# Optimization experiments

Hardware: AMD Instinct MI355X
Metric: run time of the kernel (lower is better)

The kernel has to match this reference:

```python
import jax, jax.numpy as jnp
import numpy as np

N = 100000      # nodes
E = 2500000     # edges
DIN, H, DOUT = 3, 32, 4
EPS = 1e-5

def _lin(k, i, o):
    kw, kb = jax.random.split(k)
    lim = 1.0 / np.sqrt(i)
    W = jax.random.uniform(kw, (i, o), jnp.float32, -lim, lim)
    b = jax.random.uniform(kb, (o,), jnp.float32, -lim, lim)
    return W, b

def setup_inputs():
    key = jax.random.key(0)
    ks = jax.random.split(key, 12)
    x = jax.random.normal(ks[0], (N, DIN), jnp.float32)
    edge_index = jax.random.randint(ks[1], (2, E), 0, N, dtype=jnp.int32)
    w_in1, b_in1 = _lin(ks[2], DIN, H)
    w_in2, b_in2 = _lin(ks[3], H, H)
    gamma = jnp.ones((H,), jnp.float32)
    beta = jnp.zeros((H,), jnp.float32)
    wg1, bg1 = _lin(ks[4], H, H)
    wg2, bg2 = _lin(ks[5], H, H)
    wg3, bg3 = _lin(ks[6], H, H)
    wo1, bo1 = _lin(ks[7], H, H)
    wo2, bo2 = _lin(ks[8], H, H)
    wo3, bo3 = _lin(ks[9], H, DOUT)
    return dict(x=x, w_in1=w_in1, b_in1=b_in1, w_in2=w_in2, b_in2=b_in2,
                gamma=gamma, beta=beta,
                wg1=wg1, bg1=bg1, wg2=wg2, bg2=bg2, wg3=wg3, bg3=bg3,
                wo1=wo1, bo1=bo1, wo2=wo2, bo2=bo2, wo3=wo3, bo3=bo3,
                edge_index=edge_index)

def _gcn(h, W, b, src, dst, norm):
    # PyG GCNConv: x' = scatter_add(norm * (xW)[src] -> dst) + bias
    hw = h @ W                                   # [N, H]
    msg = hw[src] * norm[:, None]                # [E+N, H] gather + scale
    out = jax.ops.segment_sum(msg, dst, num_segments=N)
    return out + b

def reference(x, w_in1, b_in1, w_in2, b_in2, gamma, beta,
              wg1, bg1, wg2, bg2, wg3, bg3,
              wo1, bo1, wo2, bo2, wo3, bo3, edge_index):
    leaky = lambda v: jax.nn.leaky_relu(v, 0.01)
    # input MLP
    h = leaky(x @ w_in1 + b_in1)
    h = leaky(h @ w_in2 + b_in2)
    # BatchNorm1d (training-mode batch statistics, biased variance)
    mu = jnp.mean(h, axis=0)
    var = jnp.mean((h - mu) ** 2, axis=0)
    h = (h - mu) * jax.lax.rsqrt(var + EPS) * gamma + beta
    # gcn_norm with self-loops: deg over target index, sym normalization
    loop = jnp.arange(N, dtype=edge_index.dtype)
    src = jnp.concatenate([edge_index[0], loop])
    dst = jnp.concatenate([edge_index[1], loop])
    deg = jax.ops.segment_sum(jnp.ones_like(src, jnp.float32), dst, num_segments=N)
    dis = jax.lax.rsqrt(deg)                     # deg >= 1 due to self-loops
    norm = dis[src] * dis[dst]                   # [E+N]
    h = jax.nn.elu(_gcn(h, wg1, bg1, src, dst, norm))
    h = jax.nn.elu(_gcn(h, wg2, bg2, src, dst, norm))
    h = jax.nn.elu(_gcn(h, wg3, bg3, src, dst, norm))
    # output MLP
    r = leaky(h @ wo1 + bo1)
    r = leaky(r @ wo2 + bo2)
    r = r @ wo3 + bo3                            # [N, 4]
    r = r.at[:, 0].set(jax.nn.sigmoid(r[:, 0]))
    return r
```

## Files before the change

### kernel.cpp

```cpp
#include <hip/hip_runtime.h>
#include <hip/hip_fp16.h>

#define HF 32
#define EPS 1e-5f
#define BSH 6
#define BSZ 64
#define CH  16384
#define SUBCAP 320
#define CAP (8*SUBCAP)
#define FXS 524288.0f
#define FXI (1.0f/524288.0f)

typedef int vi4 __attribute__((ext_vector_type(4)));

__device__ __forceinline__ float leaky(float v){ return fmaxf(v, 0.01f*v); }
__device__ __forceinline__ float elu1(float v){ return v > 0.f ? v : (expf(v)-1.f); }
__device__ __forceinline__ float sigmoidf(float v){ return 1.f/(1.f+expf(-v)); }

__device__ __forceinline__ int4 nt_load_i4(const int* p){
    vi4 v = __builtin_nontemporal_load((const vi4*)p);
    return make_int4(v.x, v.y, v.z, v.w);
}

__device__ __forceinline__ void accum8_fx(int* a, float4 v){
    const __half2* p = (const __half2*)&v;
#pragma unroll
    for (int k = 0; k < 4; k++){
        float2 f = __half22float2(p[k]);
        atomicAdd(a + 2*k,     __float2int_rn(f.x * FXS));
        atomicAdd(a + 2*k + 1, __float2int_rn(f.y * FXS));
    }
}

union SMem {
    struct {
        float sW1[3*HF]; float sB1[HF]; float sW2[HF*HF]; float sB2[HF];
        float sh[256][33];
    } mlp;
    struct { int lcnt[2048]; int lbase[2048]; int lpos[2048]; } bin;
};

__global__ __launch_bounds__(256)
void k_mlp_bin(const float* __restrict__ x,
               const float* __restrict__ w1, const float* __restrict__ b1,
               const float* __restrict__ w2, const float* __restrict__ b2,
               __half* __restrict__ h, float* __restrict__ stats,
               const int* __restrict__ src, const int* __restrict__ dst,
               int* __restrict__ gfill, int* __restrict__ ep,
               int N, int E, int B, int NC){
    __shared__ SMem sm;
    int t = threadIdx.x;
    if ((int)blockIdx.x < NC){
        int bid = blockIdx.x;
        for (int i = t; i < B; i += 256){ sm.bin.lcnt[i] = 0; sm.bin.lpos[i] = 0; }
        __syncthreads();
        int base = bid * CH;
        int xcd = bid & 7;
        bool full = (base + CH <= E);
        if (full){
            for (int i = 0; i < 16; i++){
                int4 d4 = nt_load_i4(dst + base + (t + i*256)*4);
                atomicAdd(&sm.bin.lcnt[d4.x >> BSH], 1);
                atomicAdd(&sm.bin.lcnt[d4.y >> BSH], 1);
                atomicAdd(&sm.bin.lcnt[d4.z >> BSH], 1);
                atomicAdd(&sm.bin.lcnt[d4.w >> BSH], 1);
            }
        } else {
            for (int i = 0; i < 64; i++){
                int e = base + t + i*256;
                if (e < E) atomicAdd(&sm.bin.lcnt[dst[e] >> BSH], 1);
            }
        }
        __syncthreads();
        for (int i = t; i < B; i += 256){
            int c = sm.bin.lcnt[i];
            sm.bin.lbase[i] = c ? (i*CAP + xcd*SUBCAP + atomicAdd(&gfill[i*8 + xcd], c)) : 0;
        }
        __syncthreads();
        if (full){
            for (int i = 0; i < 16; i++){
                int idx = base + (t + i*256)*4;
                int4 d4 = *(const int4*)(dst + idx);
                int4 s4 = *(const int4*)(src + idx);
                int dd[4] = {d4.x, d4.y, d4.z, d4.w};
                int ss[4] = {s4.x, s4.y, s4.z, s4.w};
#pragma unroll
                for (int k = 0; k < 4; k++){
                    int bb = dd[k] >> BSH;
                    int p = sm.bin.lbase[bb] + atomicAdd(&sm.bin.lpos[bb], 1);
                    ep[p] = (ss[k] << BSH) | (dd[k] & (BSZ-1));
                }
            }
        } else {
            for (int i = 0; i < 64; i++){
                int e = base + t + i*256;
                if (e < E){
                    int d = dst[e], s = src[e];
                    int bb = d >> BSH;
                    int p = sm.bin.lbase[bb] + atomicAdd(&sm.bin.lpos[bb], 1);
                    ep[p] = (s << BSH) | (d & (BSZ-1));
                }
            }
        }
    } else {
        for (int i = t; i < 3*HF; i += 256) sm.mlp.sW1[i] = w1[i];
        if (t < HF){ sm.mlp.sB1[t] = b1[t]; sm.mlp.sB2[t] = b2[t]; }
        for (int i = t; i < HF*HF; i += 256) sm.mlp.sW2[i] = w2[i];
        __syncthreads();
        int n = (blockIdx.x - NC)*256 + t;
        float h2[HF];
        if (n < N){
            float x0 = x[(size_t)n*3], x1 = x[(size_t)n*3+1], x2 = x[(size_t)n*3+2];
            float h1[HF];
#pragma unroll
            for (int j = 0; j < HF; j++){
                float v = fmaf(x0, sm.mlp.sW1[j], fmaf(x1, sm.mlp.sW1[HF+j],
                          fmaf(x2, sm.mlp.sW1[2*HF+j], sm.mlp.sB1[j])));
                h1[j] = leaky(v);
            }
#pragma unroll
            for (int j = 0; j < HF; j++){
                float v = sm.mlp.sB2[j];
#pragma unroll
                for (int i = 0; i < HF; i++) v = fmaf(h1[i], sm.mlp.sW2[i*HF+j], v);
                h2[j] = leaky(v);
            }
            float4* hv = (float4*)(h + (size_t)n*HF);
#pragma unroll
            for (int jb = 0; jb < 4; jb++){
                __half2 hh[4];
#pragma unroll
                for (int k = 0; k < 4; k++)
                    hh[k] = __float22half2_rn(make_float2(h2[jb*8+2*k], h2[jb*8+2*k+1]));
                hv[jb] = *(float4*)hh;
            }
        } else {
#pragma unroll
            for (int j = 0; j < HF; j++) h2[j] = 0.f;
        }
#pragma unroll
        for (int j = 0; j < HF; j++) sm.mlp.sh[t][j] = h2[j];
        __syncthreads();
        int f = t & 31, g = t >> 5;
        float s = 0.f, ss = 0.f;
        for (int i = 0; i < 32; i++){
            float v = sm.mlp.sh[g*32 + i][f];
            s += v; ss += v*v;
        }
        __syncthreads();
        sm.mlp.sh[g][f] = s; sm.mlp.sh[8+g][f] = ss;
        __syncthreads();
        if (t < HF){
            float a = 0.f, b = 0.f;
#pragma unroll
            for (int g2 = 0; g2 < 8; g2++){ a += sm.mlp.sh[g2][t]; b += sm.mlp.sh[8+g2][t]; }
            atomicAdd(&stats[t], a);
            atomicAdd(&stats[HF+t], b);
        }
    }
}

__global__ __launch_bounds__(256)
void k_deg_t1(int* __restrict__ ep, const int* __restrict__ gfill,
              int* __restrict__ bcnt, float* __restrict__ dis,
              const __half* __restrict__ h, const float* __restrict__ stats,
              const float* __restrict__ gamma, const float* __restrict__ beta,
              const float* __restrict__ W, __half* __restrict__ tout,
              int N, int B){
    __shared__ union { int sep[CAP]; float hsh[BSZ][HF+1]; } u;
    __shared__ int lcnt[BSZ];
    __shared__ float sW[HF*HF];
    __shared__ float sscale[HF], sshift[HF];
    int t = threadIdx.x;
    int b = blockIdx.x;
    for (int i = t; i < HF*HF; i += 256) sW[i] = W[i];
    if (t < HF){
        float inv = 1.0f/(float)N;
        float mu  = stats[t]*inv;
        float var = stats[HF+t]*inv - mu*mu;
        float rs  = rsqrtf(var + EPS);
        float sc  = rs*gamma[t];
        sscale[t] = sc;
        sshift[t] = beta[t] - mu*sc;
    }
    if (t < BSZ) lcnt[t] = 0;
    int cx[8], coff[8], cnt = 0;
#pragma unroll
    for (int xx = 0; xx < 8; xx++){ cx[xx] = gfill[b*8 + xx]; coff[xx] = cnt; cnt += cx[xx]; }
    int base = b*CAP;
    __syncthreads();
#pragma unroll
    for (int xx = 0; xx < 8; xx++)
        for (int j = t; j < cx[xx]; j += 256) u.sep[coff[xx] + j] = ep[base + xx*SUBCAP + j];
    __syncthreads();
    for (int e = t; e < cnt; e += 256) atomicAdd(&lcnt[u.sep[e] & (BSZ-1)], 1);
    for (int e = t; e < cnt; e += 256) ep[base + e] = u.sep[e];
    if (t == 0) bcnt[b] = cnt;
    __syncthreads();
    int nloc = t >> 2, q = t & 3;
    int n = b*BSZ + nloc;
    float dloc = 0.f;
    if (n < N){
        dloc = rsqrtf((float)lcnt[nloc] + 1.0f);
        if (q == 0) dis[n] = dloc;
        float4 raw = ((const float4*)h)[(size_t)n*4 + q];
        const __half2* p2 = (const __half2*)&raw;
#pragma unroll
        for (int k = 0; k < 4; k++){
            float2 f2 = __half22float2(p2[k]);
            int f = 8*q + 2*k;
            u.hsh[nloc][f]   = fmaf(f2.x, sscale[f],   sshift[f]);
            u.hsh[nloc][f+1] = fmaf(f2.y, sscale[f+1], sshift[f+1]);
        }
    }
    __syncthreads();
    if (n < N){
        int fo = 8*q;
        float o[8] = {0.f,0.f,0.f,0.f,0.f,0.f,0.f,0.f};
#pragma unroll
        for (int i = 0; i < HF; i++){
            float vi = u.hsh[nloc][i];
            float4 w0 = *(const float4*)&sW[i*HF + fo];
            float4 w1 = *(const float4*)&sW[i*HF + fo + 4];
            o[0] = fmaf(vi, w0.x, o[0]); o[1] = fmaf(vi, w0.y, o[1]);
            o[2] = fmaf(vi, w0.z, o[2]); o[3] = fmaf(vi, w0.w, o[3]);
            o[4] = fmaf(vi, w1.x, o[4]); o[5] = fmaf(vi, w1.y, o[5]);
            o[6] = fmaf(vi, w1.z, o[6]); o[7] = fmaf(vi, w1.w, o[7]);
        }
        __half2 hh[4];
#pragma unroll
        for (int k = 0; k < 4; k++)
            hh[k] = __float22half2_rn(make_float2(o[2*k]*dloc, o[2*k+1]*dloc));
        ((float4*)tout)[(size_t)n*4 + q] = *(float4*)hh;
    }
}

__global__ __launch_bounds__(256)
void k_gather_t(const __half* __restrict__ tin, const int* __restrict__ ep,
                const int* __restrict__ bcnt, const float* __restrict__ dis,
                const float* __restrict__ bias, const float* __restrict__ W,
                __half* __restrict__ tout, int N){
    __shared__ int iacc[BSZ][HF+1];
    __shared__ float sW[HF*HF];
    float* facc = (float*)iacc;
    int t = threadIdx.x, b = blockIdx.x;
    for (int i = t; i < HF*HF; i += 256) sW[i] = W[i];
    for (int i = t; i < BSZ*(HF+1); i += 256) ((int*)iacc)[i] = 0;
    int cnt = bcnt[b];
    int base = b*CAP;
    __syncthreads();
    int g = t >> 2, l = t & 3;
    const float4* tv = (const float4*)tin;
    int j = g;
    for (; j + 64 < cnt; j += 128){
        int p0 = ep[base + j], p1 = ep[base + j + 64];
        float4 r0 = tv[(size_t)(p0 >> BSH)*4 + l];
        float4 r1 = tv[(size_t)(p1 >> BSH)*4 + l];
        accum8_fx(&iacc[p0 & (BSZ-1)][8*l], r0);
        accum8_fx(&iacc[p1 & (BSZ-1)][8*l], r1);
    }
    for (; j < cnt; j += 64){
        int p0 = ep[base + j];
        float4 r0 = tv[(size_t)(p0 >> BSH)*4 + l];
        accum8_fx(&iacc[p0 & (BSZ-1)][8*l], r0);
    }
    __syncthreads();
    int nloc = t >> 2, q = t & 3;
    int n = b*BSZ + nloc;
    float dv = 0.f;
    float fin[8];
    if (n < N){
        dv = dis[n];
        float4 s0 = tv[(size_t)n*4 + q];
        const __half2* ph = (const __half2*)&s0;
#pragma unroll
        for (int k = 0; k < 4; k++){
            float2 f2 = __half22float2(ph[k]);
            int f = 8*q + 2*k;
            float a0 = (float)iacc[nloc][f]   * FXI + f2.x;
            float a1 = (float)iacc[nloc][f+1] * FXI + f2.y;
            fin[2*k]   = elu1(fmaf(dv, a0, bias[f]));
            fin[2*k+1] = elu1(fmaf(dv, a1, bias[f+1]));
        }
    }
    __syncthreads();
    if (n < N){
#pragma unroll
        for (int k = 0; k < 8; k++) facc[nloc*(HF+1) + 8*q + k] = fin[k];
    }
    __syncthreads();
    if (n < N){
        int fo = 8*q;
        float o[8] = {0.f,0.f,0.f,0.f,0.f,0.f,0.f,0.f};
#pragma unroll
        for (int i = 0; i < HF; i++){
            float hv = facc[nloc*(HF+1) + i];
            float4 w0 = *(const float4*)&sW[i*HF + fo];
            float4 w1 = *(const float4*)&sW[i*HF + fo + 4];
            o[0] = fmaf(hv, w0.x, o[0]); o[1] = fmaf(hv, w0.y, o[1]);
            o[2] = fmaf(hv, w0.z, o[2]); o[3] = fmaf(hv, w0.w, o[3]);
            o[4] = fmaf(hv, w1.x, o[4]); o[5] = fmaf(hv, w1.y, o[5]);
            o[6] = fmaf(hv, w1.z, o[6]); o[7] = fmaf(hv, w1.w, o[7]);
        }
        __half2 hh[4];
#pragma unroll
        for (int k = 0; k < 4; k++)
            hh[k] = __float22half2_rn(make_float2(o[2*k]*dv, o[2*k+1]*dv));
        ((float4*)tout)[(size_t)n*4 + q] = *(float4*)hh;
    }
}

__global__ __launch_bounds__(256)
void k_gather_out(const __half* __restrict__ tin, const int* __restrict__ ep,
                  const int* __restrict__ bcnt, const float* __restrict__ dis,
                  const float* __restrict__ bg3,
                  const float* __restrict__ wo1, const float* __restrict__ bo1,
                  const float* __restrict__ wo2, const float* __restrict__ bo2,
                  const float* __restrict__ wo3, const float* __restrict__ bo3,
                  float* __restrict__ out, int N){
    __shared__ int iacc[BSZ][HF+1];
    __shared__ float sW1[HF*HF], sW2[HF*HF], sW3[HF*4];
    float* facc = (float*)iacc;
    int t = threadIdx.x, b = blockIdx.x;
    for (int i = t; i < HF*HF; i += 256){ sW1[i] = wo1[i]; sW2[i] = wo2[i]; }
    if (t < HF*4) sW3[t] = wo3[t];
    for (int i = t; i < BSZ*(HF+1); i += 256) ((int*)iacc)[i] = 0;
    int cnt = bcnt[b];
    int base = b*CAP;
    __syncthreads();
    int g = t >> 2, l = t & 3;
    const float4* tv = (const float4*)tin;
    int j = g;
    for (; j + 64 < cnt; j += 128){
        int p0 = ep[base + j], p1 = ep[base + j + 64];
        float4 r0 = tv[(size_t)(p0 >> BSH)*4 + l];
        float4 r1 = tv[(size_t)(p1 >> BSH)*4 + l];
        accum8_fx(&iacc[p0 & (BSZ-1)][8*l], r0);
        accum8_fx(&iacc[p1 & (BSZ-1)][8*l], r1);
    }
    for (; j < cnt; j += 64){
        int p0 = ep[base + j];
        float4 r0 = tv[(size_t)(p0 >> BSH)*4 + l];
        accum8_fx(&iacc[p0 & (BSZ-1)][8*l], r0);
    }
    __syncthreads();
    int nloc = t >> 2, q = t & 3;
    int n = b*BSZ + nloc;
    float fin[8];
    if (n < N){
        float dv = dis[n];
        float4 s0 = tv[(size_t)n*4 + q];
        const __half2* ph = (const __half2*)&s0;
#pragma unroll
        for (int k = 0; k < 4; k++){
            float2 f2 = __half22float2(ph[k]);
            int f = 8*q + 2*k;
            float a0 = (float)iacc[nloc][f]   * FXI + f2.x;
            float a1 = (float)iacc[nloc][f+1] * FXI + f2.y;
            fin[2*k]   = elu1(fmaf(dv, a0, bg3[f]));
            fin[2*k+1] = elu1(fmaf(dv, a1, bg3[f+1]));
        }
    }
    __syncthreads();
    if (n < N){
#pragma unroll
        for (int k = 0; k < 8; k++) facc[nloc*(HF+1) + 8*q + k] = fin[k];
    }
    __syncthreads();
    float o1[8];
    if (n < N){
        int fo = 8*q;
#pragma unroll
        for (int c = 0; c < 8; c++) o1[c] = bo1[fo + c];
#pragma unroll
        for (int i = 0; i < HF; i++){
            float hv = facc[nloc*(HF+1) + i];
            float4 w0 = *(const float4*)&sW1[i*HF + fo];
            float4 w1 = *(const float4*)&sW1[i*HF + fo + 4];
            o1[0] = fmaf(hv, w0.x, o1[0]); o1[1] = fmaf(hv, w0.y, o1[1]);
            o1[2] = fmaf(hv, w0.z, o1[2]); o1[3] = fmaf(hv, w0.w, o1[3]);
            o1[4] = fmaf(hv, w1.x, o1[4]); o1[5] = fmaf(hv, w1.y, o1[5]);
            o1[6] = fmaf(hv, w1.z, o1[6]); o1[7] = fmaf(hv, w1.w, o1[7]);
        }
    }
    __syncthreads();
    if (n < N){
        int fo = 8*q;
#pragma unroll
        for (int c = 0; c < 8; c++) facc[nloc*(HF+1) + fo + c] = leaky(o1[c]);
    }
    __syncthreads();
    float o2[8];
    if (n < N){
        int fo = 8*q;
#pragma unroll
        for (int c = 0; c < 8; c++) o2[c] = bo2[fo + c];
#pragma unroll
        for (int i = 0; i < HF; i++){
            float hv = facc[nloc*(HF+1) + i];
            float4 w0 = *(const float4*)&sW2[i*HF + fo];
            float4 w1 = *(const float4*)&sW2[i*HF + fo + 4];
            o2[0] = fmaf(hv, w0.x, o2[0]); o2[1] = fmaf(hv, w0.y, o2[1]);
            o2[2] = fmaf(hv, w0.z, o2[2]); o2[3] = fmaf(hv, w0.w, o2[3]);
            o2[4] = fmaf(hv, w1.x, o2[4]); o2[5] = fmaf(hv, w1.y, o2[5]);
            o2[6] = fmaf(hv, w1.z, o2[6]); o2[7] = fmaf(hv, w1.w, o2[7]);
        }
    }
    __syncthreads();
    if (n < N){
        int fo = 8*q;
#pragma unroll
        for (int c = 0; c < 8; c++) facc[nloc*(HF+1) + fo + c] = leaky(o2[c]);
    }
    __syncthreads();
    if (n < N){
        float v = bo3[q];
#pragma unroll
        for (int i = 0; i < HF; i++) v = fmaf(facc[nloc*(HF+1) + i], sW3[i*4 + q], v);
        if (q == 0) v = sigmoidf(v);
        out[(size_t)n*4 + q] = v;
    }
}

extern "C" void kernel_launch(void* const* d_in, const int* in_sizes, int n_in,
                              void* d_out, int out_size, void* d_ws, size_t ws_size,
                              hipStream_t stream) {
    const float* x     = (const float*)d_in[0];
    const float* w_in1 = (const float*)d_in[1];
    const float* b_in1 = (const float*)d_in[2];
    const float* w_in2 = (const float*)d_in[3];
    const float* b_in2 = (const float*)d_in[4];
    const float* gamma = (const float*)d_in[5];
    const float* beta  = (const float*)d_in[6];
    const float* wg1   = (const float*)d_in[7];
    const float* bg1   = (const float*)d_in[8];
    const float* wg2   = (const float*)d_in[9];
    const float* bg2   = (const float*)d_in[10];
    const float* wg3   = (const float*)d_in[11];
    const float* bg3   = (const float*)d_in[12];
    const float* wo1   = (const float*)d_in[13];
    const float* bo1   = (const float*)d_in[14];
    const float* wo2   = (const float*)d_in[15];
    const float* bo2   = (const float*)d_in[16];
    const float* wo3   = (const float*)d_in[17];
    const float* bo3   = (const float*)d_in[18];
    const int*   ei    = (const int*)d_in[19];

    int N = in_sizes[0] / 3;
    int E = in_sizes[19] / 2;
    int B = (N + BSZ - 1) >> BSH;

    char* w = (char*)d_ws;
    size_t o = 0;
    auto alloc = [&](size_t bytes){ size_t r = o; o = (o + bytes + 255) & ~(size_t)255; return r; };
    float* stats = (float*)(w + alloc(2*HF*sizeof(float)));
    int*   gfill = (int*)  (w + alloc((size_t)B*8*4));
    size_t zero_bytes = o;
    int*   bcnt  = (int*)  (w + alloc((size_t)B*4));
    float* dis   = (float*)(w + alloc((size_t)N*4));
    int*   ep    = (int*)  (w + alloc((size_t)B*CAP*4));
    __half* bufH = (__half*)(w + alloc((size_t)N*HF*2));
    __half* tA   = (__half*)(w + alloc((size_t)N*HF*2));
    __half* tB   = (__half*)(w + alloc((size_t)N*HF*2));

    hipMemsetAsync(d_ws, 0, zero_bytes, stream);

    const int* src = ei;
    const int* dst = ei + E;
    int NB1 = (N + 255) / 256;
    int NC  = (E + CH - 1) / CH;

    k_mlp_bin<<<NC + NB1, 256, 0, stream>>>(x, w_in1, b_in1, w_in2, b_in2, bufH, stats,
                                            src, dst, gfill, ep, N, E, B, NC);
    k_deg_t1<<<B, 256, 0, stream>>>(ep, gfill, bcnt, dis,
                                    bufH, stats, gamma, beta, wg1, tA, N, B);
    k_gather_t<<<B, 256, 0, stream>>>(tA, ep, bcnt, dis, bg1, wg2, tB, N);
    k_gather_t<<<B, 256, 0, stream>>>(tB, ep, bcnt, dis, bg2, wg3, tA, N);
    k_gather_out<<<B, 256, 0, stream>>>(tA, ep, bcnt, dis, bg3,
                                        wo1, bo1, wo2, bo2, wo3, bo3, (float*)d_out, N);
}
```

Measured before the change: 277.4 us.

## Drop edge-list compaction; gather directly from per-XCD sub-segments and halve bin chunk

The degree kernel no longer copies the binned edge list through shared memory and writes it back compacted. Instead, each gather kernel walks the eight per-XCD sub-segments directly, using the gfill counts, which removes the bcnt buffer and an extra read/write pass over the edge list. The binning chunk size is also halved, giving twice as many binning blocks. In exchange, gather loops now have eight shorter inner loops with more tail iterations per block.

```diff
diff --git a/kernel.cpp b/kernel.cpp
--- a/kernel.cpp
+++ b/kernel.cpp
@@ -5,7 +5,7 @@
 #define EPS 1e-5f
 #define BSH 6
 #define BSZ 64
-#define CH  16384
+#define CH  8192
 #define SUBCAP 320
 #define CAP (8*SUBCAP)
 #define FXS 524288.0f
@@ -58,7 +58,7 @@
         int xcd = bid & 7;
         bool full = (base + CH <= E);
         if (full){
-            for (int i = 0; i < 16; i++){
+            for (int i = 0; i < 8; i++){
                 int4 d4 = nt_load_i4(dst + base + (t + i*256)*4);
                 atomicAdd(&sm.bin.lcnt[d4.x >> BSH], 1);
                 atomicAdd(&sm.bin.lcnt[d4.y >> BSH], 1);
@@ -66,7 +66,7 @@
                 atomicAdd(&sm.bin.lcnt[d4.w >> BSH], 1);
             }
         } else {
-            for (int i = 0; i < 64; i++){
+            for (int i = 0; i < 32; i++){
                 int e = base + t + i*256;
                 if (e < E) atomicAdd(&sm.bin.lcnt[dst[e] >> BSH], 1);
             }
@@ -78,7 +78,7 @@
         }
         __syncthreads();
         if (full){
-            for (int i = 0; i < 16; i++){
+            for (int i = 0; i < 8; i++){
                 int idx = base + (t + i*256)*4;
                 int4 d4 = *(const int4*)(dst + idx);
                 int4 s4 = *(const int4*)(src + idx);
@@ -92,7 +92,7 @@
                 }
             }
         } else {
-            for (int i = 0; i < 64; i++){
+            for (int i = 0; i < 32; i++){
                 int e = base + t + i*256;
                 if (e < E){
                     int d = dst[e], s = src[e];
@@ -161,14 +161,14 @@
 }
 
 __global__ __launch_bounds__(256)
-void k_deg_t1(int* __restrict__ ep, const int* __restrict__ gfill,
-              int* __restrict__ bcnt, float* __restrict__ dis,
+void k_deg_t1(const int* __restrict__ ep, const int* __restrict__ gfill,
+              float* __restrict__ dis,
               const __half* __restrict__ h, const float* __restrict__ stats,
               const float* __restrict__ gamma, const float* __restrict__ beta,
               const float* __restrict__ W, __half* __restrict__ tout,
               int N, int B){
-    __shared__ union { int sep[CAP]; float hsh[BSZ][HF+1]; } u;
     __shared__ int lcnt[BSZ];
+    __shared__ float hsh[BSZ][HF+1];
     __shared__ float sW[HF*HF];
     __shared__ float sscale[HF], sshift[HF];
     int t = threadIdx.x;
@@ -184,18 +184,14 @@
         sshift[t] = beta[t] - mu*sc;
     }
     if (t < BSZ) lcnt[t] = 0;
-    int cx[8], coff[8], cnt = 0;
-#pragma unroll
-    for (int xx = 0; xx < 8; xx++){ cx[xx] = gfill[b*8 + xx]; coff[xx] = cnt; cnt += cx[xx]; }
     int base = b*CAP;
     __syncthreads();
 #pragma unroll
-    for (int xx = 0; xx < 8; xx++)
-        for (int j = t; j < cx[xx]; j += 256) u.sep[coff[xx] + j] = ep[base + xx*SUBCAP + j];
-    __syncthreads();
-    for (int e = t; e < cnt; e += 256) atomicAdd(&lcnt[u.sep[e] & (BSZ-1)], 1);
-    for (int e = t; e < cnt; e += 256) ep[base + e] = u.sep[e];
-    if (t == 0) bcnt[b] = cnt;
+    for (int x = 0; x < 8; x++){
+        int cx = gfill[b*8 + x];
+        const int* seg = ep + base + x*SUBCAP;
+        for (int j = t; j < cx; j += 256) atomicAdd(&lcnt[seg[j] & (BSZ-1)], 1);
+    }
     __syncthreads();
     int nloc = t >> 2, q = t & 3;
     int n = b*BSZ + nloc;
@@ -209,8 +205,8 @@
         for (int k = 0; k < 4; k++){
             float2 f2 = __half22float2(p2[k]);
             int f = 8*q + 2*k;
-            u.hsh[nloc][f]   = fmaf(f2.x, sscale[f],   sshift[f]);
-            u.hsh[nloc][f+1] = fmaf(f2.y, sscale[f+1], sshift[f+1]);
+            hsh[nloc][f]   = fmaf(f2.x, sscale[f],   sshift[f]);
+            hsh[nloc][f+1] = fmaf(f2.y, sscale[f+1], sshift[f+1]);
         }
     }
     __syncthreads();
@@ -219,7 +215,7 @@
         float o[8] = {0.f,0.f,0.f,0.f,0.f,0.f,0.f,0.f};
 #pragma unroll
         for (int i = 0; i < HF; i++){
-            float vi = u.hsh[nloc][i];
+            float vi = hsh[nloc][i];
             float4 w0 = *(const float4*)&sW[i*HF + fo];
             float4 w1 = *(const float4*)&sW[i*HF + fo + 4];
             o[0] = fmaf(vi, w0.x, o[0]); o[1] = fmaf(vi, w0.y, o[1]);
@@ -237,7 +233,7 @@
 
 __global__ __launch_bounds__(256)
 void k_gather_t(const __half* __restrict__ tin, const int* __restrict__ ep,
-                const int* __restrict__ bcnt, const float* __restrict__ dis,
+                const int* __restrict__ gfill, const float* __restrict__ dis,
                 const float* __restrict__ bias, const float* __restrict__ W,
                 __half* __restrict__ tout, int N){
     __shared__ int iacc[BSZ][HF+1];
@@ -246,23 +242,27 @@
     int t = threadIdx.x, b = blockIdx.x;
     for (int i = t; i < HF*HF; i += 256) sW[i] = W[i];
     for (int i = t; i < BSZ*(HF+1); i += 256) ((int*)iacc)[i] = 0;
-    int cnt = bcnt[b];
     int base = b*CAP;
     __syncthreads();
     int g = t >> 2, l = t & 3;
     const float4* tv = (const float4*)tin;
-    int j = g;
-    for (; j + 64 < cnt; j += 128){
-        int p0 = ep[base + j], p1 = ep[base + j + 64];
-        float4 r0 = tv[(size_t)(p0 >> BSH)*4 + l];
-        float4 r1 = tv[(size_t)(p1 >> BSH)*4 + l];
-        accum8_fx(&iacc[p0 & (BSZ-1)][8*l], r0);
-        accum8_fx(&iacc[p1 & (BSZ-1)][8*l], r1);
-    }
-    for (; j < cnt; j += 64){
-        int p0 = ep[base + j];
-        float4 r0 = tv[(size_t)(p0 >> BSH)*4 + l];
-        accum8_fx(&iacc[p0 & (BSZ-1)][8*l], r0);
+#pragma unroll
+    for (int x = 0; x < 8; x++){
+        int cx = gfill[b*8 + x];
+        const int* seg = ep + base + x*SUBCAP;
+        int j = g;
+        for (; j + 64 < cx; j += 128){
+            int p0 = seg[j], p1 = seg[j + 64];
+            float4 r0 = tv[(size_t)(p0 >> BSH)*4 + l];
+            float4 r1 = tv[(size_t)(p1 >> BSH)*4 + l];
+            accum8_fx(&iacc[p0 & (BSZ-1)][8*l], r0);
+            accum8_fx(&iacc[p1 & (BSZ-1)][8*l], r1);
+        }
+        for (; j < cx; j += 64){
+            int p0 = seg[j];
+            float4 r0 = tv[(size_t)(p0 >> BSH)*4 + l];
+            accum8_fx(&iacc[p0 & (BSZ-1)][8*l], r0);
+        }
     }
     __syncthreads();
     int nloc = t >> 2, q = t & 3;
@@ -312,7 +312,7 @@
 
 __global__ __launch_bounds__(256)
 void k_gather_out(const __half* __restrict__ tin, const int* __restrict__ ep,
-                  const int* __restrict__ bcnt, const float* __restrict__ dis,
+                  const int* __restrict__ gfill, const float* __restrict__ dis,
                   const float* __restrict__ bg3,
                   const float* __restrict__ wo1, const float* __restrict__ bo1,
                   const float* __restrict__ wo2, const float* __restrict__ bo2,
@@ -325,23 +325,27 @@
     for (int i = t; i < HF*HF; i += 256){ sW1[i] = wo1[i]; sW2[i] = wo2[i]; }
     if (t < HF*4) sW3[t] = wo3[t];
     for (int i = t; i < BSZ*(HF+1); i += 256) ((int*)iacc)[i] = 0;
-    int cnt = bcnt[b];
     int base = b*CAP;
     __syncthreads();
     int g = t >> 2, l = t & 3;
     const float4* tv = (const float4*)tin;
-    int j = g;
-    for (; j + 64 < cnt; j += 128){
-        int p0 = ep[base + j], p1 = ep[base + j + 64];
-        float4 r0 = tv[(size_t)(p0 >> BSH)*4 + l];
-        float4 r1 = tv[(size_t)(p1 >> BSH)*4 + l];
-        accum8_fx(&iacc[p0 & (BSZ-1)][8*l], r0);
-        accum8_fx(&iacc[p1 & (BSZ-1)][8*l], r1);
-    }
-    for (; j < cnt; j += 64){
-        int p0 = ep[base + j];
-        float4 r0 = tv[(size_t)(p0 >> BSH)*4 + l];
-        accum8_fx(&iacc[p0 & (BSZ-1)][8*l], r0);
+#pragma unroll
+    for (int x = 0; x < 8; x++){
+        int cx = gfill[b*8 + x];
+        const int* seg = ep + base + x*SUBCAP;
+        int j = g;
+        for (; j + 64 < cx; j += 128){
+            int p0 = seg[j], p1 = seg[j + 64];
+            float4 r0 = tv[(size_t)(p0 >> BSH)*4 + l];
+            float4 r1 = tv[(size_t)(p1 >> BSH)*4 + l];
+            accum8_fx(&iacc[p0 & (BSZ-1)][8*l], r0);
+            accum8_fx(&iacc[p1 & (BSZ-1)][8*l], r1);
+        }
+        for (; j < cx; j += 64){
+            int p0 = seg[j];
+            float4 r0 = tv[(size_t)(p0 >> BSH)*4 + l];
+            accum8_fx(&iacc[p0 & (BSZ-1)][8*l], r0);
+        }
     }
     __syncthreads();
     int nloc = t >> 2, q = t & 3;
@@ -456,7 +460,6 @@
     float* stats = (float*)(w + alloc(2*HF*sizeof(float)));
     int*   gfill = (int*)  (w + alloc((size_t)B*8*4));
     size_t zero_bytes = o;
-    int*   bcnt  = (int*)  (w + alloc((size_t)B*4));
     float* dis   = (float*)(w + alloc((size_t)N*4));
     int*   ep    = (int*)  (w + alloc((size_t)B*CAP*4));
     __half* bufH = (__half*)(w + alloc((size_t)N*HF*2));
@@ -472,10 +475,10 @@
 
     k_mlp_bin<<<NC + NB1, 256, 0, stream>>>(x, w_in1, b_in1, w_in2, b_in2, bufH, stats,
                                             src, dst, gfill, ep, N, E, B, NC);
-    k_deg_t1<<<B, 256, 0, stream>>>(ep, gfill, bcnt, dis,
+    k_deg_t1<<<B, 256, 0, stream>>>(ep, gfill, dis,
                                     bufH, stats, gamma, beta, wg1, tA, N, B);
-    k_gather_t<<<B, 256, 0, stream>>>(tA, ep, bcnt, dis, bg1, wg2, tB, N);
-    k_gather_t<<<B, 256, 0, stream>>>(tB, ep, bcnt, dis, bg2, wg3, tA, N);
-    k_gather_out<<<B, 256, 0, stream>>>(tA, ep, bcnt, dis, bg3,
+    k_gather_t<<<B, 256, 0, stream>>>(tA, ep, gfill, dis, bg1, wg2, tB, N);
+    k_gather_t<<<B, 256, 0, stream>>>(tB, ep, gfill, dis, bg2, wg3, tA, N);
+    k_gather_out<<<B, 256, 0, stream>>>(tA, ep, gfill, dis, bg3,
                                         wo1, bo1, wo2, bo2, wo3, bo3, (float*)d_out, N);
 }
```

After: 283.1 us. +2.1%, slower.
